# Performance work log

Hardware: AMD Instinct MI355X
Metric: run time of the kernel (lower is better)

The kernel has to match this reference:

```python
import jax, jax.numpy as jnp
import numpy as np

NUM_USERS = 100000
NUM_ITEMS = 50000
NUM_OTHERS = 20000
N_NODES = NUM_USERS + NUM_ITEMS + NUM_OTHERS
LATENT_DIM = 64
N_LAYERS = 3
NNZ = 5000000
BATCH = 8192


def setup_inputs() -> dict:
    key = jax.random.key(0)
    ks = jax.random.split(key, 8)
    user_emb = jax.random.normal(ks[0], (NUM_USERS, LATENT_DIM), dtype=jnp.float32) * 0.1
    item_emb = jax.random.normal(ks[1], (NUM_ITEMS, LATENT_DIM), dtype=jnp.float32) * 0.1
    other_emb = jax.random.normal(ks[2], (NUM_OTHERS, LATENT_DIM), dtype=jnp.float32) * 0.1
    # normalized-adjacency-like positive values (symmetric norm values are small positives)
    vals = jax.random.uniform(ks[3], (NNZ,), dtype=jnp.float32) * 0.02
    row_idx = jax.random.randint(ks[4], (NNZ,), 0, N_NODES, dtype=jnp.int64 if jax.config.jax_enable_x64 else jnp.int32)
    col_idx = jax.random.randint(ks[5], (NNZ,), 0, N_NODES, dtype=jnp.int64 if jax.config.jax_enable_x64 else jnp.int32)
    users = jax.random.randint(ks[6], (BATCH,), 0, NUM_USERS, dtype=jnp.int32)
    items = jax.random.randint(ks[7], (BATCH,), 0, NUM_ITEMS, dtype=jnp.int32)
    return {
        "user_emb": user_emb,
        "item_emb": item_emb,
        "other_emb": other_emb,
        "vals": vals,
        "row_idx": row_idx,
        "col_idx": col_idx,
        "users": users,
        "items": items,
    }


def _spmm(vals, row_idx, col_idx, x):
    # sparse.mm(A, x): out[r] = sum_{(r,c) in A} vals * x[c]
    gathered = vals[:, None] * x[col_idx]  # [nnz, d]
    return jax.ops.segment_sum(gathered, row_idx, num_segments=N_NODES)


def reference(user_emb, item_emb, other_emb, vals, row_idx, col_idx, users, items):
    all_emb = jnp.concatenate([user_emb, item_emb, other_emb], axis=0)  # [N, d]
    acc = all_emb
    cur = all_emb
    for _ in range(N_LAYERS):
        cur = _spmm(vals, row_idx, col_idx, cur)
        acc = acc + cur
    lgn_out = acc / jnp.float32(N_LAYERS + 1)  # mean over stacked layer embeddings
    all_users = lgn_out[:NUM_USERS]
    all_items = lgn_out[NUM_USERS:NUM_USERS + NUM_ITEMS]
    users_embs = all_users[users]  # [B, d]
    items_embs = all_items[items]  # [B, d]
    gamma = jnp.sum(users_embs * items_embs, axis=1)  # [B]
    return gamma
```

## Files before the change

kernel.cpp:

```cpp
#include <hip/hip_runtime.h>

#define NUM_USERS 100000
#define NUM_ITEMS 50000
#define NUM_OTHERS 20000
#define N_NODES 170000
#define DIM 64
#define NNZ 5000000
#define BATCH 8192

#define BSHIFT 10
#define RPB (1 << BSHIFT)
#define NBUCK ((N_NODES + RPB - 1) / RPB)
#define COLMASK 0x3FFFF
#define BCAPSHIFT 15
#define BCAP (1 << BCAPSHIFT)
#define NBLK 512
#define SBS 1024
#define CHUNK ((NNZ + NBLK - 1) / NBLK)

typedef float f32x2 __attribute__((ext_vector_type(2)));

static __device__ __forceinline__ unsigned f2bf(float f) {
    unsigned u = __float_as_uint(f);
    u = (u + 0x7fff + ((u >> 16) & 1)) >> 16;
    return u;
}
static __device__ __forceinline__ float bflo(unsigned u) {
    return __uint_as_float(u << 16);
}
static __device__ __forceinline__ float bfhi(unsigned u) {
    return __uint_as_float(u & 0xFFFF0000u);
}

__global__ void build_cur0(const float* __restrict__ ue,
                           const float* __restrict__ ie,
                           const float* __restrict__ oe,
                           ushort4* __restrict__ cur) {
    const int total = N_NODES * (DIM / 4);
    for (int i = blockIdx.x * blockDim.x + threadIdx.x; i < total;
         i += gridDim.x * blockDim.x) {
        const int node = i >> 4;
        const int sub  = i & 15;
        const float* src;
        if (node < NUM_USERS)                  src = ue + (size_t)node * DIM;
        else if (node < NUM_USERS + NUM_ITEMS) src = ie + (size_t)(node - NUM_USERS) * DIM;
        else                                   src = oe + (size_t)(node - NUM_USERS - NUM_ITEMS) * DIM;
        const float4 f = reinterpret_cast<const float4*>(src)[sub];
        ushort4 o;
        o.x = (unsigned short)f2bf(f.x); o.y = (unsigned short)f2bf(f.y);
        o.z = (unsigned short)f2bf(f.z); o.w = (unsigned short)f2bf(f.w);
        cur[i] = o;
    }
}

__global__ void init_acc(const int* __restrict__ users,
                         const int* __restrict__ items,
                         const float* __restrict__ ue,
                         const float* __restrict__ ie,
                         float4* __restrict__ uacc,
                         float4* __restrict__ iacc) {
    const int total = BATCH * (DIM / 4);
    int i = blockIdx.x * blockDim.x + threadIdx.x;
    if (i >= total) return;
    const int b = i >> 4;
    const int sub = i & 15;
    uacc[i] = reinterpret_cast<const float4*>(ue + (size_t)users[b] * DIM)[sub];
    iacc[i] = reinterpret_cast<const float4*>(ie + (size_t)items[b] * DIM)[sub];
}

__global__ __launch_bounds__(SBS) void bucket_scatter(const int* __restrict__ rows,
                                                      const int* __restrict__ cols,
                                                      const float* __restrict__ vals,
                                                      int* __restrict__ bucket_cnt,
                                                      int2* __restrict__ bkt) {
    __shared__ int h[NBUCK];
    __shared__ int base[NBUCK];
    for (int i = threadIdx.x; i < NBUCK; i += SBS) h[i] = 0;
    __syncthreads();
    const int s = blockIdx.x * CHUNK;
    const int e = min(s + CHUNK, NNZ);
    for (int i = s + threadIdx.x; i < e; i += SBS)
        atomicAdd(&h[rows[i] >> BSHIFT], 1);
    __syncthreads();
    for (int i = threadIdx.x; i < NBUCK; i += SBS)
        base[i] = h[i] ? atomicAdd(&bucket_cnt[i], h[i]) : 0;
    __syncthreads();
    for (int i = threadIdx.x; i < NBUCK; i += SBS) h[i] = 0;
    __syncthreads();
    for (int i = s + threadIdx.x; i < e; i += SBS) {
        const int r  = rows[i];
        const int bk = r >> BSHIFT;
        const int lr = r & (RPB - 1);
        const int pos = base[bk] + atomicAdd(&h[bk], 1);
        bkt[((size_t)bk << BCAPSHIFT) + pos] = make_int2((lr << 18) | cols[i],
                                                         __float_as_int(vals[i]));
    }
}

__global__ __launch_bounds__(1024) void bucket_to_csr(const int* __restrict__ bucket_cnt,
                                                      const int2* __restrict__ bkt,
                                                      unsigned* __restrict__ rowinfo,
                                                      int2* __restrict__ packed) {
    __shared__ int cnt[RPB];
    __shared__ int rs[RPB];
    __shared__ int scan[RPB];
    const int k = blockIdx.x;
    const int rbase = k << BSHIFT;
    const int nvalid = min(RPB, N_NODES - rbase);
    const int n = bucket_cnt[k];
    const int2* __restrict__ src = bkt + ((size_t)k << BCAPSHIFT);
    int2* __restrict__ dst = packed + ((size_t)k << BCAPSHIFT);
    const int t = threadIdx.x;

    cnt[t] = 0;
    __syncthreads();
    for (int i = t; i < n; i += 1024)
        atomicAdd(&cnt[src[i].x >> 18], 1);
    __syncthreads();

    const int v = cnt[t];
    int acc = v;
    scan[t] = v;
    __syncthreads();
    for (int off = 1; off < 1024; off <<= 1) {
        const int add = (t >= off) ? scan[t - off] : 0;
        __syncthreads();
        acc += add;
        scan[t] = acc;
        __syncthreads();
    }
    const int excl = acc - v;
    rs[t] = excl;
    if (t < nvalid)
        rowinfo[rbase + t] = ((unsigned)((k << BCAPSHIFT) + excl) << 8) | (unsigned)v;
    __syncthreads();

    for (int i = t; i < n; i += 1024) {
        const int2 pk = src[i];
        const int lr = pk.x >> 18;
        const int pos = atomicAdd(&rs[lr], 1);
        dst[pos] = make_int2((pk.x & COLMASK) << 7, pk.y);
    }
}

static __device__ __forceinline__ void spmm_row_accum(
        const unsigned long long* __restrict__ packed,
        const unsigned short* __restrict__ x,
        int s, int e, int g, int d8b,
        f32x2& a0, f32x2& a1, f32x2& a2, f32x2& a3) {
    const char* xb = (const char*)x;
    for (int i = s; i < e; i += 32) {
        const int j0 = i + g;
        const int j1 = j0 + 8;
        const int j2 = j0 + 16;
        const int j3 = j0 + 24;
        const unsigned long long p0 = __builtin_nontemporal_load(packed + j0);
        const unsigned long long p1 = __builtin_nontemporal_load(packed + j1);
        const unsigned long long p2 = __builtin_nontemporal_load(packed + j2);
        const unsigned long long p3 = __builtin_nontemporal_load(packed + j3);
        const unsigned c0 = ((j0 < e) ? (unsigned)(p0 & 0xFFFFFFFFu) : 0u) + d8b;
        const unsigned c1 = ((j1 < e) ? (unsigned)(p1 & 0xFFFFFFFFu) : 0u) + d8b;
        const unsigned c2 = ((j2 < e) ? (unsigned)(p2 & 0xFFFFFFFFu) : 0u) + d8b;
        const unsigned c3 = ((j3 < e) ? (unsigned)(p3 & 0xFFFFFFFFu) : 0u) + d8b;
        const float v0 = (j0 < e) ? __uint_as_float((unsigned)(p0 >> 32)) : 0.f;
        const float v1 = (j1 < e) ? __uint_as_float((unsigned)(p1 >> 32)) : 0.f;
        const float v2 = (j2 < e) ? __uint_as_float((unsigned)(p2 >> 32)) : 0.f;
        const float v3 = (j3 < e) ? __uint_as_float((unsigned)(p3 >> 32)) : 0.f;
        const uint4 x0 = *reinterpret_cast<const uint4*>(xb + c0);
        const uint4 x1 = *reinterpret_cast<const uint4*>(xb + c1);
        const uint4 x2 = *reinterpret_cast<const uint4*>(xb + c2);
        const uint4 x3 = *reinterpret_cast<const uint4*>(xb + c3);
        const f32x2 w0 = {v0, v0}, w1 = {v1, v1}, w2 = {v2, v2}, w3 = {v3, v3};
        a0 += w0 * (f32x2){bflo(x0.x), bfhi(x0.x)};
        a1 += w0 * (f32x2){bflo(x0.y), bfhi(x0.y)};
        a2 += w0 * (f32x2){bflo(x0.z), bfhi(x0.z)};
        a3 += w0 * (f32x2){bflo(x0.w), bfhi(x0.w)};
        a0 += w1 * (f32x2){bflo(x1.x), bfhi(x1.x)};
        a1 += w1 * (f32x2){bflo(x1.y), bfhi(x1.y)};
        a2 += w1 * (f32x2){bflo(x1.z), bfhi(x1.z)};
        a3 += w1 * (f32x2){bflo(x1.w), bfhi(x1.w)};
        a0 += w2 * (f32x2){bflo(x2.x), bfhi(x2.x)};
        a1 += w2 * (f32x2){bflo(x2.y), bfhi(x2.y)};
        a2 += w2 * (f32x2){bflo(x2.z), bfhi(x2.z)};
        a3 += w2 * (f32x2){bflo(x2.w), bfhi(x2.w)};
        a0 += w3 * (f32x2){bflo(x3.x), bfhi(x3.x)};
        a1 += w3 * (f32x2){bflo(x3.y), bfhi(x3.y)};
        a2 += w3 * (f32x2){bflo(x3.z), bfhi(x3.z)};
        a3 += w3 * (f32x2){bflo(x3.w), bfhi(x3.w)};
    }
}

static __device__ __forceinline__ void butterfly8(f32x2& a0, f32x2& a1,
                                                  f32x2& a2, f32x2& a3) {
    #pragma unroll
    for (int off = 8; off < 64; off <<= 1) {
        a0.x += __shfl_xor(a0.x, off); a0.y += __shfl_xor(a0.y, off);
        a1.x += __shfl_xor(a1.x, off); a1.y += __shfl_xor(a1.y, off);
        a2.x += __shfl_xor(a2.x, off); a2.y += __shfl_xor(a2.y, off);
        a3.x += __shfl_xor(a3.x, off); a3.y += __shfl_xor(a3.y, off);
    }
}

__global__ __launch_bounds__(256) void spmm_csr8(const unsigned* __restrict__ rowinfo,
                                                 const unsigned long long* __restrict__ packed,
                                                 const unsigned short* __restrict__ x,
                                                 unsigned short* __restrict__ y) {
    const int row  = blockIdx.x * 4 + (threadIdx.x >> 6);
    const int lane = threadIdx.x & 63;
    if (row >= N_NODES) return;
    const unsigned info = rowinfo[row];
    const int s = (int)(info >> 8);
    const int e = s + (int)(info & 0xFFu);
    const int g   = lane >> 3;
    const int d8b = (lane & 7) * 16;

    f32x2 a0 = {0, 0}, a1 = {0, 0}, a2 = {0, 0}, a3 = {0, 0};
    spmm_row_accum(packed, x, s, e, g, d8b, a0, a1, a2, a3);
    butterfly8(a0, a1, a2, a3);

    if (lane < 8) {
        uint4 o;
        o.x = f2bf(a0.x) | (f2bf(a0.y) << 16);
        o.y = f2bf(a1.x) | (f2bf(a1.y) << 16);
        o.z = f2bf(a2.x) | (f2bf(a2.y) << 16);
        o.w = f2bf(a3.x) | (f2bf(a3.y) << 16);
        *reinterpret_cast<uint4*>(y + (size_t)row * DIM + lane * 8) = o;
    }
}

__global__ __launch_bounds__(256) void spmm_batch_final8(const unsigned* __restrict__ rowinfo,
                                                         const unsigned long long* __restrict__ packed,
                                                         const unsigned short* __restrict__ x,
                                                         const int* __restrict__ users,
                                                         const int* __restrict__ items,
                                                         float* __restrict__ uacc,
                                                         float* __restrict__ iacc) {
    const int w    = blockIdx.x * 4 + (threadIdx.x >> 6);
    const int lane = threadIdx.x & 63;
    if (w >= 2 * BATCH) return;
    const int b = w >> 1;
    const int isItem = w & 1;
    const int row = isItem ? (NUM_USERS + items[b]) : users[b];
    const unsigned info = rowinfo[row];
    const int s = (int)(info >> 8);
    const int e = s + (int)(info & 0xFFu);
    const int g   = lane >> 3;
    const int d8b = (lane & 7) * 16;

    f32x2 a0 = {0, 0}, a1 = {0, 0}, a2 = {0, 0}, a3 = {0, 0};
    spmm_row_accum(packed, x, s, e, g, d8b, a0, a1, a2, a3);
    butterfly8(a0, a1, a2, a3);

    if (lane < 8) {
        float* dst = (isItem ? iacc : uacc) + (size_t)b * DIM + lane * 8;
        float4 q0 = reinterpret_cast<float4*>(dst)[0];
        float4 q1 = reinterpret_cast<float4*>(dst)[1];
        q0.x += a0.x; q0.y += a0.y; q0.z += a1.x; q0.w += a1.y;
        q1.x += a2.x; q1.y += a2.y; q1.z += a3.x; q1.w += a3.y;
        reinterpret_cast<float4*>(dst)[0] = q0;
        reinterpret_cast<float4*>(dst)[1] = q1;
    }
}

__global__ void gather_add(const int* __restrict__ users,
                           const int* __restrict__ items,
                           const unsigned short* __restrict__ y,
                           float4* __restrict__ uacc,
                           float4* __restrict__ iacc) {
    const int total = BATCH * (DIM / 4);
    int i = blockIdx.x * blockDim.x + threadIdx.x;
    if (i >= total) return;
    const int b = i >> 4;
    const int sub = i & 15;
    const int un = users[b];
    const int in = NUM_USERS + items[b];
    float4 a = uacc[i];
    const ushort4 yu = *reinterpret_cast<const ushort4*>(y + (size_t)un * DIM + sub * 4);
    a.x += bflo(yu.x); a.y += bflo(yu.y); a.z += bflo(yu.z); a.w += bflo(yu.w);
    uacc[i] = a;
    float4 c = iacc[i];
    const ushort4 yi = *reinterpret_cast<const ushort4*>(y + (size_t)in * DIM + sub * 4);
    c.x += bflo(yi.x); c.y += bflo(yi.y); c.z += bflo(yi.z); c.w += bflo(yi.w);
    iacc[i] = c;
}

__global__ void dot_out(const float* __restrict__ uacc,
                        const float* __restrict__ iacc,
                        float* __restrict__ gamma) {
    const int b = blockIdx.x * (blockDim.x / 64) + (threadIdx.x / 64);
    const int lane = threadIdx.x & 63;
    if (b >= BATCH) return;
    float p = uacc[b * DIM + lane] * iacc[b * DIM + lane];
    #pragma unroll
    for (int off = 32; off > 0; off >>= 1) p += __shfl_down(p, off);
    if (lane == 0) gamma[b] = p * 0.0625f;
}

extern "C" void kernel_launch(void* const* d_in, const int* in_sizes, int n_in,
                              void* d_out, int out_size, void* d_ws, size_t ws_size,
                              hipStream_t stream) {
    const float* ue    = (const float*)d_in[0];
    const float* ie    = (const float*)d_in[1];
    const float* oe    = (const float*)d_in[2];
    const float* vals  = (const float*)d_in[3];
    const int*   rows  = (const int*)d_in[4];
    const int*   cols  = (const int*)d_in[5];
    const int*   users = (const int*)d_in[6];
    const int*   items = (const int*)d_in[7];
    float* out = (float*)d_out;

    char* p = (char*)d_ws;
    int2* bkt = (int2*)p;
    unsigned short* cur = (unsigned short*)p;
    p += ((size_t)NBUCK << BCAPSHIFT) * sizeof(int2);
    unsigned short* nxt = (unsigned short*)p;
    p += (size_t)N_NODES * DIM * sizeof(unsigned short);
    int2* packed = (int2*)p;
    p += (((size_t)NBUCK << BCAPSHIFT) + 64) * sizeof(int2);
    unsigned* rowinfo = (unsigned*)p;  p += (size_t)(N_NODES + 4) * sizeof(unsigned);
    int* bucket_cnt = (int*)p;  p += (size_t)(NBUCK + 4) * sizeof(int);
    float* uacc = (float*)p;  p += (size_t)BATCH * DIM * sizeof(float);
    float* iacc = (float*)p;  p += (size_t)BATCH * DIM * sizeof(float);

    hipMemsetAsync(bucket_cnt, 0, (size_t)NBUCK * sizeof(int), stream);
    bucket_scatter<<<NBLK, SBS, 0, stream>>>(rows, cols, vals, bucket_cnt, bkt);
    bucket_to_csr<<<NBUCK, 1024, 0, stream>>>(bucket_cnt, bkt, rowinfo, packed);

    build_cur0<<<2048, 256, 0, stream>>>(ue, ie, oe, (ushort4*)cur);
    init_acc<<<(BATCH * 16 + 255) / 256, 256, 0, stream>>>(users, items, ue, ie,
                                                           (float4*)uacc, (float4*)iacc);

    for (int layer = 0; layer < 2; ++layer) {
        spmm_csr8<<<(N_NODES + 3) / 4, 256, 0, stream>>>(rowinfo,
                                                         (const unsigned long long*)packed,
                                                         cur, nxt);
        gather_add<<<(BATCH * 16 + 255) / 256, 256, 0, stream>>>(users, items, nxt,
                                                                 (float4*)uacc, (float4*)iacc);
        unsigned short* t = cur; cur = nxt; nxt = t;
    }

    spmm_batch_final8<<<(2 * BATCH) / 4 + 1, 256, 0, stream>>>(rowinfo,
                                                               (const unsigned long long*)packed,
                                                               cur, users, items, uacc, iacc);

    dot_out<<<BATCH / 4, 256, 0, stream>>>(uacc, iacc, out);
}
```

Baseline: 324.6 us.

## Fuse init and gather-add kernels into SpMM launches and stage bucket scatter in LDS

The build_cur0 and init_acc kernels are merged into one launch. Each layer's gather_add is folded into the next SpMM launch as extra blocks, and the last one into the final batch kernel, so the layer accumulation now reads the previous layer's embeddings. bucket_scatter now sorts each chunk by bucket in shared memory using a prefix scan, then writes it out contiguously, aiming for coalesced global writes instead of scattered ones. The changes cut kernel launches and scattered stores, at the cost of a large LDS stage buffer (about 78KB) that may limit occupancy, plus a binary search per element.

```diff
diff --git a/kernel.cpp b/kernel.cpp
--- a/kernel.cpp
+++ b/kernel.cpp
@@ -15,8 +15,10 @@
 #define BCAPSHIFT 15
 #define BCAP (1 << BCAPSHIFT)
 #define NBLK 512
-#define SBS 1024
+#define SSBS 1024
 #define CHUNK ((NNZ + NBLK - 1) / NBLK)
+#define SPMM_BLOCKS ((N_NODES + 3) / 4)
+#define GADD_BLOCKS ((BATCH * 16) / 256)
 
 typedef float f32x2 __attribute__((ext_vector_type(2)));
 
@@ -32,68 +34,97 @@
     return __uint_as_float(u & 0xFFFF0000u);
 }
 
-__global__ void build_cur0(const float* __restrict__ ue,
-                           const float* __restrict__ ie,
-                           const float* __restrict__ oe,
-                           ushort4* __restrict__ cur) {
-    const int total = N_NODES * (DIM / 4);
-    for (int i = blockIdx.x * blockDim.x + threadIdx.x; i < total;
-         i += gridDim.x * blockDim.x) {
-        const int node = i >> 4;
-        const int sub  = i & 15;
-        const float* src;
-        if (node < NUM_USERS)                  src = ue + (size_t)node * DIM;
-        else if (node < NUM_USERS + NUM_ITEMS) src = ie + (size_t)(node - NUM_USERS) * DIM;
-        else                                   src = oe + (size_t)(node - NUM_USERS - NUM_ITEMS) * DIM;
-        const float4 f = reinterpret_cast<const float4*>(src)[sub];
-        ushort4 o;
-        o.x = (unsigned short)f2bf(f.x); o.y = (unsigned short)f2bf(f.y);
-        o.z = (unsigned short)f2bf(f.z); o.w = (unsigned short)f2bf(f.w);
-        cur[i] = o;
-    }
-}
-
-__global__ void init_acc(const int* __restrict__ users,
-                         const int* __restrict__ items,
-                         const float* __restrict__ ue,
-                         const float* __restrict__ ie,
-                         float4* __restrict__ uacc,
-                         float4* __restrict__ iacc) {
-    const int total = BATCH * (DIM / 4);
-    int i = blockIdx.x * blockDim.x + threadIdx.x;
-    if (i >= total) return;
-    const int b = i >> 4;
-    const int sub = i & 15;
-    uacc[i] = reinterpret_cast<const float4*>(ue + (size_t)users[b] * DIM)[sub];
-    iacc[i] = reinterpret_cast<const float4*>(ie + (size_t)items[b] * DIM)[sub];
-}
-
-__global__ __launch_bounds__(SBS) void bucket_scatter(const int* __restrict__ rows,
-                                                      const int* __restrict__ cols,
-                                                      const float* __restrict__ vals,
-                                                      int* __restrict__ bucket_cnt,
-                                                      int2* __restrict__ bkt) {
+__global__ void build_cur0_init(const float* __restrict__ ue,
+                                const float* __restrict__ ie,
+                                const float* __restrict__ oe,
+                                ushort4* __restrict__ cur,
+                                const int* __restrict__ users,
+                                const int* __restrict__ items,
+                                float4* __restrict__ uacc,
+                                float4* __restrict__ iacc) {
+    if (blockIdx.x < 2048) {
+        const int total = N_NODES * (DIM / 4);
+        for (int i = blockIdx.x * 256 + threadIdx.x; i < total; i += 2048 * 256) {
+            const int node = i >> 4;
+            const int sub  = i & 15;
+            const float* src;
+            if (node < NUM_USERS)                  src = ue + (size_t)node * DIM;
+            else if (node < NUM_USERS + NUM_ITEMS) src = ie + (size_t)(node - NUM_USERS) * DIM;
+            else                                   src = oe + (size_t)(node - NUM_USERS - NUM_ITEMS) * DIM;
+            const float4 f = reinterpret_cast<const float4*>(src)[sub];
+            ushort4 o;
+            o.x = (unsigned short)f2bf(f.x); o.y = (unsigned short)f2bf(f.y);
+            o.z = (unsigned short)f2bf(f.z); o.w = (unsigned short)f2bf(f.w);
+            cur[i] = o;
+        }
+    } else {
+        const int i = (blockIdx.x - 2048) * 256 + threadIdx.x;
+        const int b = i >> 4;
+        const int sub = i & 15;
+        uacc[i] = reinterpret_cast<const float4*>(ue + (size_t)users[b] * DIM)[sub];
+        iacc[i] = reinterpret_cast<const float4*>(ie + (size_t)items[b] * DIM)[sub];
+    }
+}
+
+__global__ __launch_bounds__(SSBS) void bucket_scatter(const int* __restrict__ rows,
+                                                       const int* __restrict__ cols,
+                                                       const float* __restrict__ vals,
+                                                       int* __restrict__ bucket_cnt,
+                                                       int2* __restrict__ bkt) {
+    __shared__ int2 stage[CHUNK];
     __shared__ int h[NBUCK];
-    __shared__ int base[NBUCK];
-    for (int i = threadIdx.x; i < NBUCK; i += SBS) h[i] = 0;
-    __syncthreads();
+    __shared__ int lstart[NBUCK + 1];
+    __shared__ int lcur[NBUCK];
+    __shared__ int gbias[NBUCK];
+    __shared__ int scanbuf[256];
+    const int t = threadIdx.x;
     const int s = blockIdx.x * CHUNK;
     const int e = min(s + CHUNK, NNZ);
-    for (int i = s + threadIdx.x; i < e; i += SBS)
+    const int n = e - s;
+
+    for (int i = t; i < NBUCK; i += SSBS) h[i] = 0;
+    __syncthreads();
+    for (int i = s + t; i < e; i += SSBS)
         atomicAdd(&h[rows[i] >> BSHIFT], 1);
     __syncthreads();
-    for (int i = threadIdx.x; i < NBUCK; i += SBS)
-        base[i] = h[i] ? atomicAdd(&bucket_cnt[i], h[i]) : 0;
-    __syncthreads();
-    for (int i = threadIdx.x; i < NBUCK; i += SBS) h[i] = 0;
-    __syncthreads();
-    for (int i = s + threadIdx.x; i < e; i += SBS) {
+
+    int v = 0;
+    if (t < 256) { v = (t < NBUCK) ? h[t] : 0; scanbuf[t] = v; }
+    __syncthreads();
+    int acc = v;
+    for (int off = 1; off < 256; off <<= 1) {
+        int add = 0;
+        if (t < 256 && t >= off) add = scanbuf[t - off];
+        __syncthreads();
+        if (t < 256) { acc += add; scanbuf[t] = acc; }
+        __syncthreads();
+    }
+    if (t < NBUCK) {
+        const int excl = acc - v;
+        lstart[t] = excl;
+        lcur[t]   = excl;
+        const int gb = v ? atomicAdd(&bucket_cnt[t], v) : 0;
+        gbias[t] = gb - excl;
+    }
+    if (t == 0) lstart[NBUCK] = n;
+    __syncthreads();
+
+    for (int i = s + t; i < e; i += SSBS) {
         const int r  = rows[i];
         const int bk = r >> BSHIFT;
-        const int lr = r & (RPB - 1);
-        const int pos = base[bk] + atomicAdd(&h[bk], 1);
-        bkt[((size_t)bk << BCAPSHIFT) + pos] = make_int2((lr << 18) | cols[i],
-                                                         __float_as_int(vals[i]));
+        const int pos = atomicAdd(&lcur[bk], 1);
+        stage[pos] = make_int2(((r & (RPB - 1)) << 18) | cols[i],
+                               __float_as_int(vals[i]));
+    }
+    __syncthreads();
+
+    for (int i = t; i < n; i += SSBS) {
+        int lo = 0, hi = NBUCK;
+        while (hi - lo > 1) {
+            const int mid = (lo + hi) >> 1;
+            if (lstart[mid] <= i) lo = mid; else hi = mid;
+        }
+        bkt[((size_t)lo << BCAPSHIFT) + gbias[lo] + i] = stage[i];
     }
 }
 
@@ -204,7 +235,27 @@
 __global__ __launch_bounds__(256) void spmm_csr8(const unsigned* __restrict__ rowinfo,
                                                  const unsigned long long* __restrict__ packed,
                                                  const unsigned short* __restrict__ x,
-                                                 unsigned short* __restrict__ y) {
+                                                 unsigned short* __restrict__ y,
+                                                 const int* __restrict__ users,
+                                                 const int* __restrict__ items,
+                                                 float4* __restrict__ uacc4,
+                                                 float4* __restrict__ iacc4) {
+    if (blockIdx.x >= SPMM_BLOCKS) {
+        const int i = (blockIdx.x - SPMM_BLOCKS) * 256 + threadIdx.x;
+        const int b = i >> 4;
+        const int sub = i & 15;
+        const int un = users[b];
+        const int in = NUM_USERS + items[b];
+        float4 a = uacc4[i];
+        const ushort4 yu = *reinterpret_cast<const ushort4*>(x + (size_t)un * DIM + sub * 4);
+        a.x += bflo(yu.x); a.y += bflo(yu.y); a.z += bflo(yu.z); a.w += bflo(yu.w);
+        uacc4[i] = a;
+        float4 c = iacc4[i];
+        const ushort4 yi = *reinterpret_cast<const ushort4*>(x + (size_t)in * DIM + sub * 4);
+        c.x += bflo(yi.x); c.y += bflo(yi.y); c.z += bflo(yi.z); c.w += bflo(yi.w);
+        iacc4[i] = c;
+        return;
+    }
     const int row  = blockIdx.x * 4 + (threadIdx.x >> 6);
     const int lane = threadIdx.x & 63;
     if (row >= N_NODES) return;
@@ -252,36 +303,18 @@
     butterfly8(a0, a1, a2, a3);
 
     if (lane < 8) {
+        const ushort4 xa = *reinterpret_cast<const ushort4*>(x + (size_t)row * DIM + lane * 8);
+        const ushort4 xc = *reinterpret_cast<const ushort4*>(x + (size_t)row * DIM + lane * 8 + 4);
         float* dst = (isItem ? iacc : uacc) + (size_t)b * DIM + lane * 8;
         float4 q0 = reinterpret_cast<float4*>(dst)[0];
         float4 q1 = reinterpret_cast<float4*>(dst)[1];
-        q0.x += a0.x; q0.y += a0.y; q0.z += a1.x; q0.w += a1.y;
-        q1.x += a2.x; q1.y += a2.y; q1.z += a3.x; q1.w += a3.y;
+        q0.x += a0.x + bflo(xa.x); q0.y += a0.y + bflo(xa.y);
+        q0.z += a1.x + bflo(xa.z); q0.w += a1.y + bflo(xa.w);
+        q1.x += a2.x + bflo(xc.x); q1.y += a2.y + bflo(xc.y);
+        q1.z += a3.x + bflo(xc.z); q1.w += a3.y + bflo(xc.w);
         reinterpret_cast<float4*>(dst)[0] = q0;
         reinterpret_cast<float4*>(dst)[1] = q1;
     }
-}
-
-__global__ void gather_add(const int* __restrict__ users,
-                           const int* __restrict__ items,
-                           const unsigned short* __restrict__ y,
-                           float4* __restrict__ uacc,
-                           float4* __restrict__ iacc) {
-    const int total = BATCH * (DIM / 4);
-    int i = blockIdx.x * blockDim.x + threadIdx.x;
-    if (i >= total) return;
-    const int b = i >> 4;
-    const int sub = i & 15;
-    const int un = users[b];
-    const int in = NUM_USERS + items[b];
-    float4 a = uacc[i];
-    const ushort4 yu = *reinterpret_cast<const ushort4*>(y + (size_t)un * DIM + sub * 4);
-    a.x += bflo(yu.x); a.y += bflo(yu.y); a.z += bflo(yu.z); a.w += bflo(yu.w);
-    uacc[i] = a;
-    float4 c = iacc[i];
-    const ushort4 yi = *reinterpret_cast<const ushort4*>(y + (size_t)in * DIM + sub * 4);
-    c.x += bflo(yi.x); c.y += bflo(yi.y); c.z += bflo(yi.z); c.w += bflo(yi.w);
-    iacc[i] = c;
 }
 
 __global__ void dot_out(const float* __restrict__ uacc,
@@ -323,25 +356,26 @@
     float* iacc = (float*)p;  p += (size_t)BATCH * DIM * sizeof(float);
 
     hipMemsetAsync(bucket_cnt, 0, (size_t)NBUCK * sizeof(int), stream);
-    bucket_scatter<<<NBLK, SBS, 0, stream>>>(rows, cols, vals, bucket_cnt, bkt);
+    bucket_scatter<<<NBLK, SSBS, 0, stream>>>(rows, cols, vals, bucket_cnt, bkt);
     bucket_to_csr<<<NBUCK, 1024, 0, stream>>>(bucket_cnt, bkt, rowinfo, packed);
 
-    build_cur0<<<2048, 256, 0, stream>>>(ue, ie, oe, (ushort4*)cur);
-    init_acc<<<(BATCH * 16 + 255) / 256, 256, 0, stream>>>(users, items, ue, ie,
-                                                           (float4*)uacc, (float4*)iacc);
-
-    for (int layer = 0; layer < 2; ++layer) {
-        spmm_csr8<<<(N_NODES + 3) / 4, 256, 0, stream>>>(rowinfo,
-                                                         (const unsigned long long*)packed,
-                                                         cur, nxt);
-        gather_add<<<(BATCH * 16 + 255) / 256, 256, 0, stream>>>(users, items, nxt,
-                                                                 (float4*)uacc, (float4*)iacc);
-        unsigned short* t = cur; cur = nxt; nxt = t;
-    }
-
-    spmm_batch_final8<<<(2 * BATCH) / 4 + 1, 256, 0, stream>>>(rowinfo,
-                                                               (const unsigned long long*)packed,
-                                                               cur, users, items, uacc, iacc);
+    build_cur0_init<<<2048 + GADD_BLOCKS, 256, 0, stream>>>(ue, ie, oe, (ushort4*)cur,
+                                                            users, items,
+                                                            (float4*)uacc, (float4*)iacc);
+
+    spmm_csr8<<<SPMM_BLOCKS, 256, 0, stream>>>(rowinfo,
+                                               (const unsigned long long*)packed,
+                                               cur, nxt, users, items,
+                                               (float4*)uacc, (float4*)iacc);
+
+    spmm_csr8<<<SPMM_BLOCKS + GADD_BLOCKS, 256, 0, stream>>>(rowinfo,
+                                                             (const unsigned long long*)packed,
+                                                             nxt, cur, users, items,
+                                                             (float4*)uacc, (float4*)iacc);
+
+    spmm_batch_final8<<<(2 * BATCH) / 4, 256, 0, stream>>>(rowinfo,
+                                                           (const unsigned long long*)packed,
+                                                           cur, users, items, uacc, iacc);
 
     dot_out<<<BATCH / 4, 256, 0, stream>>>(uacc, iacc, out);
 }
```

New measurement: 312.1 us. 3.8% less time.
